# Kernel tuning notes

Hardware: AMD Instinct MI355X
Metric: run time of the kernel (lower is better)

## Reference

```python
import jax, jax.numpy as jnp
import numpy as np

NEG_INF = -jnp.inf  # aggregation identity for the max-plus semifield


def setup_inputs() -> dict:
    key = jax.random.key(0)
    k1, k2, k3 = jax.random.split(key, 3)
    B, C_in, C_out, H, W, M, N = 4, 32, 32, 80, 80, 5, 5
    x = jax.random.normal(k1, (B, C_in, H, W), dtype=jnp.float32)
    w = jax.random.normal(k2, (C_out, C_in, M, N), dtype=jnp.float32) * 0.1
    bias = jax.random.normal(k3, (C_out,), dtype=jnp.float32) * 0.1
    return {"x": x, "w": w, "bias": bias}


def reference(x, w, bias):
    """Max-plus semifield conv: out[b,co,h,w] = bias[co] + sum_ci max_{m,n} (x_pad[b,ci,h+m,w+n] + w[co,ci,m,n]).

    Faithful to SemiConv2d._semi_conv with semifield = (amax, add, -inf, 0),
    but computed with a running max over the MN taps instead of materializing
    the [B, C_out, C_in, M*N, H*W] tensor the torch code builds via unfold.
    """
    B, C_in, H, W = x.shape
    C_out, _, M, N = w.shape
    # padding exactly as in _semi_conv (odd vs even kernel), fill = aggregation identity
    pt, pb = (M // 2, M // 2) if M % 2 else (M // 2 - 1, M // 2)
    pl, pr = (N // 2, N // 2) if N % 2 else (N // 2 - 1, N // 2)
    xp = jnp.pad(x, ((0, 0), (0, 0), (pt, pb), (pl, pr)), constant_values=NEG_INF)
    # running max over the M*N taps (fixed small loop, not a data-dim loop)
    acc = jnp.full((B, C_out, C_in, H, W), NEG_INF, dtype=x.dtype)
    for m in range(M):
        for n in range(N):
            patch = xp[:, :, m:m + H, n:n + W]               # [B, C_in, H, W]
            tap = patch[:, None] + w[None, :, :, m, n, None, None]  # [B, C_out, C_in, H, W]
            acc = jnp.maximum(acc, tap)
    out = jnp.sum(acc, axis=2) + bias[None, :, None, None]   # sum over C_in, add bias
    return out
```

## Files before the change

### kernel.cpp

```cpp
#include <hip/hip_runtime.h>
#include <math.h>

#define CIN  32
#define COUT 32
#define BB   4
#define HH   80
#define WW   80
#define HW   (HH * WW)
#define NOUT (BB * COUT * HW)
#define TH   16
#define NT   320

#define XPS  88
#define XPR  84
#define XPLANE (XPR * XPS)
#define XPAD_SZ (BB * CIN * XPLANE)
#define WPAD_OFF 1048576
#define WPAD_SZ (COUT * CIN * 28)
#define PART_OFF 2097152

typedef float v4f __attribute__((ext_vector_type(4)));

__device__ __forceinline__ float max3f(float a, float b, float c) {
    float d;
    asm("v_max3_f32 %0, %1, %2, %3" : "=v"(d) : "v"(a), "v"(b), "v"(c));
    return d;
}

__global__ __launch_bounds__(256) void pad_kernel(
    const float* __restrict__ x, const float* __restrict__ w,
    float* __restrict__ ws)
{
    int idx = blockIdx.x * 256 + threadIdx.x;
    int stride = gridDim.x * 256;
    for (int i = idx; i < XPAD_SZ; i += stride) {
        int c = i % XPS;
        int t = i / XPS;
        int r = t % XPR;
        int p = t / XPR;
        int gr = r - 2, gc = c - 2;
        float v = -INFINITY;
        if (gr >= 0 && gr < HH && gc >= 0 && gc < WW)
            v = x[(size_t)p * HW + gr * WW + gc];
        ws[i] = v;
    }
    for (int i = idx; i < WPAD_SZ; i += stride) {
        int q = i % 28, p = i / 28;
        ws[WPAD_OFF + i] = (q < 28 && q < 25) ? w[p * 25 + q] : 0.0f;
    }
}

template<int NP>
__global__ __launch_bounds__(NT, 7) void semiconv_kernel(
    const float* __restrict__ ws,
    const float* __restrict__ bias,
    float* __restrict__ dst)
{
    constexpr int CP = CIN / NP;
    const int tid = threadIdx.x;
    const int bh  = blockIdx.x;
    const int cp  = blockIdx.y;
    const int zz  = blockIdx.z;
    const int b    = zz / NP;
    const int part = zz % NP;
    const int ci0  = part * CP;
    const int co0  = cp * 2;

    const int ty = tid / 20, tx = tid % 20;
    const int row = bh * TH + ty;
    const int j0  = 4 * tx;

    const float* xp = ws + ((size_t)(b * CIN + ci0) * XPR + row) * XPS + j0;
    const float* wpA = ws + WPAD_OFF + ((size_t)(co0    ) * CIN + ci0) * 28;
    const float* wpB = ws + WPAD_OFF + ((size_t)(co0 + 1) * CIN + ci0) * 28;

    float sA[4] = {0.f, 0.f, 0.f, 0.f}, sB[4] = {0.f, 0.f, 0.f, 0.f};

    #pragma unroll 1
    for (int k = 0; k < CP; ++k) {
        float wA[25], wB[25];
        #pragma unroll
        for (int q = 0; q < 25; ++q) { wA[q] = wpA[q]; wB[q] = wpB[q]; }

        float xr[5][8];
        #pragma unroll
        for (int m = 0; m < 5; ++m) {
            v4f A = *(const v4f*)(xp + m * XPS);
            v4f C = *(const v4f*)(xp + m * XPS + 4);
            xr[m][0] = A.x; xr[m][1] = A.y; xr[m][2] = A.z; xr[m][3] = A.w;
            xr[m][4] = C.x; xr[m][5] = C.y; xr[m][6] = C.z; xr[m][7] = C.w;
        }

        float aA[4], aB[4];
        #pragma unroll
        for (int m = 0; m < 5; ++m) {
            #pragma unroll
            for (int j = 0; j < 4; ++j) {
                float t = max3f(xr[m][j]     + wA[5*m],
                                xr[m][j + 1] + wA[5*m + 1],
                                xr[m][j + 2] + wA[5*m + 2]);
                float u = fmaxf(xr[m][j + 3] + wA[5*m + 3],
                                xr[m][j + 4] + wA[5*m + 4]);
                aA[j] = (m == 0) ? fmaxf(t, u) : max3f(aA[j], t, u);
                t = max3f(xr[m][j]     + wB[5*m],
                          xr[m][j + 1] + wB[5*m + 1],
                          xr[m][j + 2] + wB[5*m + 2]);
                u = fmaxf(xr[m][j + 3] + wB[5*m + 3],
                          xr[m][j + 4] + wB[5*m + 4]);
                aB[j] = (m == 0) ? fmaxf(t, u) : max3f(aB[j], t, u);
            }
        }
        #pragma unroll
        for (int j = 0; j < 4; ++j) { sA[j] += aA[j]; sB[j] += aB[j]; }

        xp  += XPLANE;
        wpA += 28;
        wpB += 28;
    }

    size_t oiA = (((size_t)b * COUT + co0) * HH + row) * WW + j0;
    size_t oiB = oiA + (size_t)HW;
    v4f rA = {sA[0], sA[1], sA[2], sA[3]};
    v4f rB = {sB[0], sB[1], sB[2], sB[3]};
    float* o = dst;
    if (NP == 1) {
        float bcA = bias[co0], bcB = bias[co0 + 1];
        rA.x += bcA; rA.y += bcA; rA.z += bcA; rA.w += bcA;
        rB.x += bcB; rB.y += bcB; rB.z += bcB; rB.w += bcB;
    } else {
        o += (size_t)part * NOUT;
    }
    *(v4f*)(o + oiA) = rA;
    *(v4f*)(o + oiB) = rB;
}

template<int NP>
__global__ __launch_bounds__(256) void reduceN_kernel(
    const float* __restrict__ part, const float* __restrict__ bias,
    float* __restrict__ out)
{
    int i4 = blockIdx.x * 256 + threadIdx.x;
    const float4* p = reinterpret_cast<const float4*>(part);
    float4 r = p[i4];
    #pragma unroll
    for (int q = 1; q < NP; ++q) {
        float4 t = p[i4 + (size_t)q * (NOUT / 4)];
        r.x += t.x; r.y += t.y; r.z += t.z; r.w += t.w;
    }
    int co = (i4 / (HW / 4)) & (COUT - 1);
    float bc = bias[co];
    r.x += bc; r.y += bc; r.z += bc; r.w += bc;
    reinterpret_cast<float4*>(out)[i4] = r;
}

__global__ __launch_bounds__(256) void naive_kernel(
    const float* __restrict__ x, const float* __restrict__ w,
    const float* __restrict__ bias, float* __restrict__ out)
{
    int o = blockIdx.x * 256 + threadIdx.x;
    if (o >= NOUT) return;
    int wcol = o % WW, h = (o / WW) % HH, co = (o / HW) % COUT, b = o / (COUT * HW);
    float sum = 0.f;
    for (int ci = 0; ci < CIN; ++ci) {
        float mx = -INFINITY;
        for (int m = 0; m < 5; ++m) {
            int gr = h + m - 2;
            if (gr < 0 || gr >= HH) continue;
            for (int n = 0; n < 5; ++n) {
                int gc = wcol + n - 2;
                if (gc < 0 || gc >= WW) continue;
                float v = x[((size_t)(b * CIN + ci)) * HW + gr * WW + gc]
                        + w[((size_t)(co * CIN + ci)) * 25 + m * 5 + n];
                mx = fmaxf(mx, v);
            }
        }
        sum += mx;
    }
    out[o] = sum + bias[co];
}

extern "C" void kernel_launch(void* const* d_in, const int* in_sizes, int n_in,
                              void* d_out, int out_size, void* d_ws, size_t ws_size,
                              hipStream_t stream) {
    const float* x    = (const float*)d_in[0];
    const float* w    = (const float*)d_in[1];
    const float* bias = (const float*)d_in[2];
    float* out        = (float*)d_out;
    float* ws         = (float*)d_ws;

    const size_t need4 = (size_t)(PART_OFF + 4ull * NOUT) * sizeof(float);
    const size_t need1 = (size_t)PART_OFF * sizeof(float);

    if (ws_size >= need4) {
        pad_kernel<<<1024, 256, 0, stream>>>(x, w, ws);
        dim3 grid(HH / TH, COUT / 2, BB * 4);
        semiconv_kernel<4><<<grid, NT, 0, stream>>>(ws, bias, ws + PART_OFF);
        reduceN_kernel<4><<<NOUT / 4 / 256, 256, 0, stream>>>(ws + PART_OFF, bias, out);
    } else if (ws_size >= need1) {
        pad_kernel<<<1024, 256, 0, stream>>>(x, w, ws);
        dim3 grid(HH / TH, COUT / 2, BB);
        semiconv_kernel<1><<<grid, NT, 0, stream>>>(ws, bias, out);
    } else {
        naive_kernel<<<(NOUT + 255) / 256, 256, 0, stream>>>(x, w, bias, out);
    }
}
```

Measured before the change: 41.32 us.

## Compute four output channels per thread and split input channels eight ways

Each thread now computes four output channels instead of two, so every loaded input patch feeds twice as many channels. The input-channel split goes from four to eight partitions so the grid stays about as large, and the reduction kernel now sums eight partial buffers. The cost is a bigger partial-sum workspace, more reduction traffic and more register pressure from sixteen accumulators with an unroll of two.

```diff
diff --git a/kernel.cpp b/kernel.cpp
--- a/kernel.cpp
+++ b/kernel.cpp
@@ -46,7 +46,7 @@
     }
     for (int i = idx; i < WPAD_SZ; i += stride) {
         int q = i % 28, p = i / 28;
-        ws[WPAD_OFF + i] = (q < 28 && q < 25) ? w[p * 25 + q] : 0.0f;
+        ws[WPAD_OFF + i] = (q < 25) ? w[p * 25 + q] : 0.0f;
     }
 }
 
@@ -59,29 +59,28 @@
     constexpr int CP = CIN / NP;
     const int tid = threadIdx.x;
     const int bh  = blockIdx.x;
-    const int cp  = blockIdx.y;
+    const int cq  = blockIdx.y;
     const int zz  = blockIdx.z;
     const int b    = zz / NP;
     const int part = zz % NP;
     const int ci0  = part * CP;
-    const int co0  = cp * 2;
+    const int co0  = cq * 4;
 
     const int ty = tid / 20, tx = tid % 20;
     const int row = bh * TH + ty;
     const int j0  = 4 * tx;
 
     const float* xp = ws + ((size_t)(b * CIN + ci0) * XPR + row) * XPS + j0;
-    const float* wpA = ws + WPAD_OFF + ((size_t)(co0    ) * CIN + ci0) * 28;
-    const float* wpB = ws + WPAD_OFF + ((size_t)(co0 + 1) * CIN + ci0) * 28;
-
-    float sA[4] = {0.f, 0.f, 0.f, 0.f}, sB[4] = {0.f, 0.f, 0.f, 0.f};
-
-    #pragma unroll 1
+    const float* wp = ws + WPAD_OFF + ((size_t)co0 * CIN + ci0) * 28;
+
+    float s[4][4];
+    #pragma unroll
+    for (int c = 0; c < 4; ++c)
+        #pragma unroll
+        for (int j = 0; j < 4; ++j) s[c][j] = 0.f;
+
+    #pragma unroll 2
     for (int k = 0; k < CP; ++k) {
-        float wA[25], wB[25];
-        #pragma unroll
-        for (int q = 0; q < 25; ++q) { wA[q] = wpA[q]; wB[q] = wpB[q]; }
-
         float xr[5][8];
         #pragma unroll
         for (int m = 0; m < 5; ++m) {
@@ -91,47 +90,49 @@
             xr[m][4] = C.x; xr[m][5] = C.y; xr[m][6] = C.z; xr[m][7] = C.w;
         }
 
-        float aA[4], aB[4];
-        #pragma unroll
-        for (int m = 0; m < 5; ++m) {
+        #pragma unroll
+        for (int c = 0; c < 4; ++c) {
+            const float* wq = wp + ((size_t)c * CIN + k) * 28;
+            float wk[25];
             #pragma unroll
-            for (int j = 0; j < 4; ++j) {
-                float t = max3f(xr[m][j]     + wA[5*m],
-                                xr[m][j + 1] + wA[5*m + 1],
-                                xr[m][j + 2] + wA[5*m + 2]);
-                float u = fmaxf(xr[m][j + 3] + wA[5*m + 3],
-                                xr[m][j + 4] + wA[5*m + 4]);
-                aA[j] = (m == 0) ? fmaxf(t, u) : max3f(aA[j], t, u);
-                t = max3f(xr[m][j]     + wB[5*m],
-                          xr[m][j + 1] + wB[5*m + 1],
-                          xr[m][j + 2] + wB[5*m + 2]);
-                u = fmaxf(xr[m][j + 3] + wB[5*m + 3],
-                          xr[m][j + 4] + wB[5*m + 4]);
-                aB[j] = (m == 0) ? fmaxf(t, u) : max3f(aB[j], t, u);
+            for (int q = 0; q < 25; ++q) wk[q] = wq[q];
+
+            float a[4];
+            #pragma unroll
+            for (int m = 0; m < 5; ++m) {
+                #pragma unroll
+                for (int j = 0; j < 4; ++j) {
+                    float t = max3f(xr[m][j]     + wk[5*m],
+                                    xr[m][j + 1] + wk[5*m + 1],
+                                    xr[m][j + 2] + wk[5*m + 2]);
+                    float u = fmaxf(xr[m][j + 3] + wk[5*m + 3],
+                                    xr[m][j + 4] + wk[5*m + 4]);
+                    a[j] = (m == 0) ? fmaxf(t, u) : max3f(a[j], t, u);
+                }
             }
-        }
-        #pragma unroll
-        for (int j = 0; j < 4; ++j) { sA[j] += aA[j]; sB[j] += aB[j]; }
-
-        xp  += XPLANE;
-        wpA += 28;
-        wpB += 28;
-    }
-
-    size_t oiA = (((size_t)b * COUT + co0) * HH + row) * WW + j0;
-    size_t oiB = oiA + (size_t)HW;
-    v4f rA = {sA[0], sA[1], sA[2], sA[3]};
-    v4f rB = {sB[0], sB[1], sB[2], sB[3]};
+            #pragma unroll
+            for (int j = 0; j < 4; ++j) s[c][j] += a[j];
+        }
+        xp += XPLANE;
+    }
+
+    size_t oi = (((size_t)b * COUT + co0) * HH + row) * WW + j0;
     float* o = dst;
     if (NP == 1) {
-        float bcA = bias[co0], bcB = bias[co0 + 1];
-        rA.x += bcA; rA.y += bcA; rA.z += bcA; rA.w += bcA;
-        rB.x += bcB; rB.y += bcB; rB.z += bcB; rB.w += bcB;
+        #pragma unroll
+        for (int c = 0; c < 4; ++c) {
+            float bc = bias[co0 + c];
+            v4f r = {s[c][0] + bc, s[c][1] + bc, s[c][2] + bc, s[c][3] + bc};
+            *(v4f*)(o + oi + (size_t)c * HW) = r;
+        }
     } else {
         o += (size_t)part * NOUT;
-    }
-    *(v4f*)(o + oiA) = rA;
-    *(v4f*)(o + oiB) = rB;
+        #pragma unroll
+        for (int c = 0; c < 4; ++c) {
+            v4f r = {s[c][0], s[c][1], s[c][2], s[c][3]};
+            *(v4f*)(o + oi + (size_t)c * HW) = r;
+        }
+    }
 }
 
 template<int NP>
@@ -188,17 +189,17 @@
     float* out        = (float*)d_out;
     float* ws         = (float*)d_ws;
 
-    const size_t need4 = (size_t)(PART_OFF + 4ull * NOUT) * sizeof(float);
+    const size_t need8 = (size_t)(PART_OFF + 8ull * NOUT) * sizeof(float);
     const size_t need1 = (size_t)PART_OFF * sizeof(float);
 
-    if (ws_size >= need4) {
+    if (ws_size >= need8) {
         pad_kernel<<<1024, 256, 0, stream>>>(x, w, ws);
-        dim3 grid(HH / TH, COUT / 2, BB * 4);
-        semiconv_kernel<4><<<grid, NT, 0, stream>>>(ws, bias, ws + PART_OFF);
-        reduceN_kernel<4><<<NOUT / 4 / 256, 256, 0, stream>>>(ws + PART_OFF, bias, out);
+        dim3 grid(HH / TH, COUT / 4, BB * 8);
+        semiconv_kernel<8><<<grid, NT, 0, stream>>>(ws, bias, ws + PART_OFF);
+        reduceN_kernel<8><<<NOUT / 4 / 256, 256, 0, stream>>>(ws + PART_OFF, bias, out);
     } else if (ws_size >= need1) {
         pad_kernel<<<1024, 256, 0, stream>>>(x, w, ws);
-        dim3 grid(HH / TH, COUT / 2, BB);
+        dim3 grid(HH / TH, COUT / 4, BB);
         semiconv_kernel<1><<<grid, NT, 0, stream>>>(ws, bias, out);
     } else {
         naive_kernel<<<(NOUT + 255) / 256, 256, 0, stream>>>(x, w, bias, out);
```

After: 43.77 us. +5.9%, slower.
